# Optimization experiments

Hardware: AMD Instinct MI355X
Metric: run time of the kernel (lower is better)

The kernel has to match this reference:

```python
import jax, jax.numpy as jnp
import numpy as np

IN_FEATURES = 2048
OUT_FEATURES = 8192


def setup_inputs() -> dict:
    key = jax.random.key(0)
    k_x, k_w, k_s, k_b = jax.random.split(key, 4)
    x = jax.random.normal(k_x, (4, 2048, IN_FEATURES), dtype=jnp.float32)
    # int8 weights as produced by quantize(): values in [-128, 127]
    weight_int8 = jax.random.randint(k_w, (OUT_FEATURES, IN_FEATURES), -128, 128, dtype=jnp.int8)
    # per-output-row scale, shape [out_features, 1]
    scale = jax.random.uniform(k_s, (OUT_FEATURES, 1), dtype=jnp.float32, minval=1e-4, maxval=0.02)
    bias = jax.random.normal(k_b, (OUT_FEATURES,), dtype=jnp.float32) * 0.01
    return {"x": x, "weight_int8": weight_int8, "scale": scale, "bias": bias}


def reference(x, weight_int8, scale, bias):
    # dequantize: [out, in] int8 -> x.dtype, scaled per output row
    weight = weight_int8.astype(x.dtype) * scale.astype(x.dtype)
    # F.linear: x @ weight.T + bias
    return jnp.einsum('bsi,oi->bso', x, weight) + bias.astype(x.dtype)
```

## Files before the change

### kernel.cpp

```cpp
#include <hip/hip_runtime.h>
#include <hip/hip_bf16.h>

#define M_DIM 8192
#define N_DIM 8192
#define K_DIM 2048

#define BK 64
#define NT (K_DIM / BK)
#define SLOT_BYTES 32768

typedef float f32x4 __attribute__((ext_vector_type(4)));
typedef int   i32x4 __attribute__((ext_vector_type(4)));
typedef unsigned int u32;
typedef u32 u32x2 __attribute__((ext_vector_type(2)));
typedef u32 u32x4 __attribute__((ext_vector_type(4)));


__device__ __forceinline__ void gload16(const unsigned char* g, char* l) {
    __builtin_amdgcn_global_load_lds(
        (const __attribute__((address_space(1))) u32*)g,
        (__attribute__((address_space(3))) u32*)l, 16, 0, 0);
}

__device__ __forceinline__ u32 pack4(int a, int b, int c, int d) {
    return (u32)(a & 255) | ((u32)(b & 255) << 8) |
           ((u32)(c & 255) << 16) | ((u32)(d & 255) << 24);
}


__global__ void __launch_bounds__(256) quant_x_k(const float* __restrict__ x,
                                                 unsigned char* __restrict__ xq,
                                                 float* __restrict__ sx) {
    const int row = blockIdx.x;
    const int t = threadIdx.x;
    const float* xr = x + (size_t)row * K_DIM;
    f32x4 v0 = *((const f32x4*)xr + t * 2);
    f32x4 v1 = *((const f32x4*)xr + t * 2 + 1);
    float m = fabsf(v0[0]);
    m = fmaxf(m, fabsf(v0[1])); m = fmaxf(m, fabsf(v0[2])); m = fmaxf(m, fabsf(v0[3]));
    m = fmaxf(m, fabsf(v1[0])); m = fmaxf(m, fabsf(v1[1]));
    m = fmaxf(m, fabsf(v1[2])); m = fmaxf(m, fabsf(v1[3]));
#pragma unroll
    for (int off = 32; off >= 1; off >>= 1)
        m = fmaxf(m, __shfl_xor(m, off, 64));
    __shared__ float wmax[4];
    if ((t & 63) == 0) wmax[t >> 6] = m;
    __syncthreads();
    m = fmaxf(fmaxf(wmax[0], wmax[1]), fmaxf(wmax[2], wmax[3]));
    m = fmaxf(m, 1e-20f);
    const float rs = 127.0f / m;
    const int q0 = (int)rintf(v0[0] * rs), q1 = (int)rintf(v0[1] * rs);
    const int q2 = (int)rintf(v0[2] * rs), q3 = (int)rintf(v0[3] * rs);
    const int q4 = (int)rintf(v1[0] * rs), q5 = (int)rintf(v1[1] * rs);
    const int q6 = (int)rintf(v1[2] * rs), q7 = (int)rintf(v1[3] * rs);
    u32x2 o;
    o[0] = pack4(q0, q1, q2, q3);
    o[1] = pack4(q4, q5, q6, q7);
    *((u32x2*)(xq + (size_t)row * K_DIM) + t) = o;
    if (t == 0) sx[row] = m / 127.0f;
}


__global__ void __launch_bounds__(256) cvt_w_k(const int* __restrict__ w,
                                               unsigned char* __restrict__ wq, int n16) {
    const int stride = gridDim.x * blockDim.x;
    for (int i = blockIdx.x * blockDim.x + threadIdx.x; i < n16; i += stride) {
        const i32x4* p = (const i32x4*)w + (size_t)i * 4;
        i32x4 a = p[0], b = p[1], c = p[2], d = p[3];
        u32x4 o;
        o[0] = pack4(a[0], a[1], a[2], a[3]);
        o[1] = pack4(b[0], b[1], b[2], b[3]);
        o[2] = pack4(c[0], c[1], c[2], c[3]);
        o[3] = pack4(d[0], d[1], d[2], d[3]);
        *((u32x4*)wq + i) = o;
    }
}


__global__ void __launch_bounds__(512, 2)
gemm_i8(const unsigned char* __restrict__ Aq, const unsigned char* __restrict__ Bq,
        const float* __restrict__ sx, const float* __restrict__ sw,
        const float* __restrict__ bias, float* __restrict__ C) {
    extern __shared__ __align__(16) char ldsb[];

    const int bid = blockIdx.x;
    const int swz = (bid & 7) * 128 + (bid >> 3);
    const int rowBase = (swz >> 5) * 256;
    const int colBase = (swz & 31) * 256;

    const int t = threadIdx.x;
    const int l = t & 63;
    const int w = t >> 6;
    const int wm = w >> 2;
    const int wn = w & 3;
    const int fr = l & 15;
    const int s4 = l >> 4;

    const int sr = t >> 2;
    const int sk = (((t & 3) ^ ((sr >> 1) & 3)) * 16);
    const unsigned char* gA0 = Aq + (size_t)(rowBase + sr) * K_DIM + sk;
    const unsigned char* gA1 = Aq + (size_t)(rowBase + 128 + sr) * K_DIM + sk;
    const unsigned char* gB0 = Bq + (size_t)(colBase + sr) * K_DIM + sk;
    const unsigned char* gB1 = Bq + (size_t)(colBase + 128 + sr) * K_DIM + sk;

#define STAGE(tk) do { \
        char* _b = ldsb + ((tk) & 3) * SLOT_BYTES; \
        const int _k = (tk) * BK; \
        gload16(gA0 + _k, _b + t * 16); \
        gload16(gA1 + _k, _b + 8192 + t * 16); \
        gload16(gB0 + _k, _b + 16384 + t * 16); \
        gload16(gB1 + _k, _b + 24576 + t * 16); \
    } while (0)

    const int pc = ((s4 ^ ((fr >> 1) & 3)) * 16);
    int aoff[8], boff[4];
#pragma unroll
    for (int mi = 0; mi < 8; ++mi)
        aoff[mi] = (wm * 128 + mi * 16 + fr) * 64 + pc;
#pragma unroll
    for (int ni = 0; ni < 4; ++ni)
        boff[ni] = 16384 + (wn * 64 + ni * 16 + fr) * 64 + pc;

    i32x4 acc[8][4] = {};
    i32x4 afC[8], bf0[4], bf1[4];

#define SB    __builtin_amdgcn_sched_barrier(0)
#define BAR   __builtin_amdgcn_s_barrier()
#define P1    __builtin_amdgcn_s_setprio(1)
#define P0    __builtin_amdgcn_s_setprio(0)
#define LGKM0 asm volatile("s_waitcnt lgkmcnt(0)" ::: "memory")
#define VM8   asm volatile("s_waitcnt vmcnt(8)" ::: "memory")
#define VM4   asm volatile("s_waitcnt vmcnt(4)" ::: "memory")
#define VM0   asm volatile("s_waitcnt vmcnt(0)" ::: "memory")

#define READS_B(dst, tk) do { \
        const char* _s = ldsb + ((tk) & 3) * SLOT_BYTES; \
        _Pragma("unroll") \
        for (int ni = 0; ni < 4; ++ni) dst[ni] = *(const i32x4*)(_s + boff[ni]); \
    } while (0)
#define READS_A(tk) do { \
        const char* _s = ldsb + ((tk) & 3) * SLOT_BYTES; \
        _Pragma("unroll") \
        for (int mi = 0; mi < 8; ++mi) afC[mi] = *(const i32x4*)(_s + aoff[mi]); \
    } while (0)
#define MFMA_ALL(BREG) do { P1; \
        _Pragma("unroll") \
        for (int mi = 0; mi < 8; ++mi) \
            _Pragma("unroll") \
            for (int ni = 0; ni < 4; ++ni) \
                acc[mi][ni] = __builtin_amdgcn_mfma_i32_16x16x64_i8( \
                    afC[mi], BREG[ni], acc[mi][ni], 0, 0, 0); \
        P0; } while (0)

#define BODY(TK, BCUR, BNXT) do { \
        STAGE((TK) + 3); \
        VM8; LGKM0; SB; BAR; SB; \
        READS_B(BNXT, (TK) + 1); SB; \
        MFMA_ALL(BCUR); SB; \
        READS_A((TK) + 1); SB; \
    } while (0)

    STAGE(0); STAGE(1); STAGE(2);
    VM8; SB; BAR; SB;
    READS_B(bf0, 0); READS_A(0); SB;

#pragma unroll 1
    for (int tk = 0; tk < NT - 4; tk += 2) {
        BODY(tk, bf0, bf1);
        BODY(tk + 1, bf1, bf0);
    }
    BODY(28, bf0, bf1);
    VM4; LGKM0; SB; BAR; SB;
    READS_B(bf0, 30); SB;
    MFMA_ALL(bf1); SB;
    READS_A(30); SB;
    VM0; LGKM0; SB; BAR; SB;
    READS_B(bf1, 31); SB;
    MFMA_ALL(bf0); SB;
    READS_A(31); SB;
    MFMA_ALL(bf1);

#undef BODY
#undef MFMA_ALL
#undef READS_A
#undef READS_B
#undef STAGE

#pragma unroll
    for (int ni = 0; ni < 4; ++ni) {
        const int col = colBase + wn * 64 + ni * 16 + fr;
        const float swc = sw[col];
        const float bz = bias[col];
#pragma unroll
        for (int mi = 0; mi < 8; ++mi) {
            const int rb = rowBase + wm * 128 + mi * 16 + s4 * 4;
            i32x4 a = acc[mi][ni];
#pragma unroll
            for (int r = 0; r < 4; ++r)
                C[(size_t)(rb + r) * N_DIM + col] =
                    (float)a[r] * (sx[rb + r] * swc) + bz;
        }
    }
}


typedef int i32x4_t __attribute__((ext_vector_type(4)));
__global__ void __launch_bounds__(256) naive_k(const float* __restrict__ x,
                                               const int* __restrict__ w,
                                               const float* __restrict__ scale,
                                               const float* __restrict__ bias,
                                               float* __restrict__ out) {
    __shared__ float xs[K_DIM];
    const int m = blockIdx.x >> 5;
    const int n = ((blockIdx.x & 31) << 8) + threadIdx.x;
    for (int i = threadIdx.x; i < K_DIM; i += 256) xs[i] = x[(size_t)m * K_DIM + i];
    __syncthreads();
    const int* wr = w + (size_t)n * K_DIM;
    float acc = 0.f;
    for (int k = 0; k < K_DIM; k += 4) {
        i32x4_t v = *(const i32x4_t*)(wr + k);
        acc += xs[k]     * (float)v[0];
        acc += xs[k + 1] * (float)v[1];
        acc += xs[k + 2] * (float)v[2];
        acc += xs[k + 3] * (float)v[3];
    }
    out[(size_t)m * N_DIM + n] = acc * scale[n] + bias[n];
}


extern "C" void kernel_launch(void* const* d_in, const int* in_sizes, int n_in,
                              void* d_out, int out_size, void* d_ws, size_t ws_size,
                              hipStream_t stream) {
    const float* x     = (const float*)d_in[0];
    const int*   w8    = (const int*)d_in[1];
    const float* sw    = (const float*)d_in[2];
    const float* bias  = (const float*)d_in[3];
    float*       out   = (float*)d_out;

    const size_t xq_bytes = (size_t)M_DIM * K_DIM;
    const size_t wq_bytes = (size_t)N_DIM * K_DIM;
    const size_t need = xq_bytes + wq_bytes + (size_t)M_DIM * sizeof(float);
    if (ws_size >= need) {
        unsigned char* xq = (unsigned char*)d_ws;
        unsigned char* wq = xq + xq_bytes;
        float* sx = (float*)(wq + wq_bytes);
        hipFuncSetAttribute((const void*)gemm_i8,
                            hipFuncAttributeMaxDynamicSharedMemorySize, 131072);
        quant_x_k<<<M_DIM, 256, 0, stream>>>(x, xq, sx);
        cvt_w_k<<<2048, 256, 0, stream>>>(w8, wq, N_DIM * K_DIM / 16);
        gemm_i8<<<dim3((M_DIM / 256) * (N_DIM / 256)), 512, 131072, stream>>>(
            xq, wq, sx, sw, bias, out);
    } else {
        naive_k<<<(M_DIM * (N_DIM / 256)), 256, 0, stream>>>(x, w8, sw, bias, out);
    }
}
```

Before: 220.7 us.

## Shrink GEMM tile to 128x256 with double-buffered LDS and higher occupancy

Halves the M tile of the int8 GEMM from 256 to 128 rows, cutting per-block accumulators and LDS use. The pipeline drops from 4 LDS slots to 2, with a simpler stage/read/MFMA loop, and launch bounds now ask for 4 blocks per CU instead of 2. The aim is to raise occupancy and hide latency through more resident waves. In exchange, arithmetic intensity per block drops, global traffic for B roughly doubles, and the loop adds an extra barrier per iteration.

```diff
diff --git a/kernel.cpp b/kernel.cpp
--- a/kernel.cpp
+++ b/kernel.cpp
@@ -7,7 +7,7 @@
 
 #define BK 64
 #define NT (K_DIM / BK)
-#define SLOT_BYTES 32768
+#define SLOT_BYTES 24576
 
 typedef float f32x4 __attribute__((ext_vector_type(4)));
 typedef int   i32x4 __attribute__((ext_vector_type(4)));
@@ -77,15 +77,15 @@
 }
 
 
-__global__ void __launch_bounds__(512, 2)
+__global__ void __launch_bounds__(512, 4)
 gemm_i8(const unsigned char* __restrict__ Aq, const unsigned char* __restrict__ Bq,
         const float* __restrict__ sx, const float* __restrict__ sw,
         const float* __restrict__ bias, float* __restrict__ C) {
     extern __shared__ __align__(16) char ldsb[];
 
     const int bid = blockIdx.x;
-    const int swz = (bid & 7) * 128 + (bid >> 3);
-    const int rowBase = (swz >> 5) * 256;
+    const int swz = (bid & 7) * 256 + (bid >> 3);
+    const int rowBase = (swz >> 5) * 128;
     const int colBase = (swz & 31) * 256;
 
     const int t = threadIdx.x;
@@ -99,91 +99,75 @@
     const int sr = t >> 2;
     const int sk = (((t & 3) ^ ((sr >> 1) & 3)) * 16);
     const unsigned char* gA0 = Aq + (size_t)(rowBase + sr) * K_DIM + sk;
-    const unsigned char* gA1 = Aq + (size_t)(rowBase + 128 + sr) * K_DIM + sk;
     const unsigned char* gB0 = Bq + (size_t)(colBase + sr) * K_DIM + sk;
     const unsigned char* gB1 = Bq + (size_t)(colBase + 128 + sr) * K_DIM + sk;
 
 #define STAGE(tk) do { \
-        char* _b = ldsb + ((tk) & 3) * SLOT_BYTES; \
+        char* _b = ldsb + ((tk) & 1) * SLOT_BYTES; \
         const int _k = (tk) * BK; \
         gload16(gA0 + _k, _b + t * 16); \
-        gload16(gA1 + _k, _b + 8192 + t * 16); \
-        gload16(gB0 + _k, _b + 16384 + t * 16); \
-        gload16(gB1 + _k, _b + 24576 + t * 16); \
+        gload16(gB0 + _k, _b + 8192 + t * 16); \
+        gload16(gB1 + _k, _b + 16384 + t * 16); \
     } while (0)
 
     const int pc = ((s4 ^ ((fr >> 1) & 3)) * 16);
-    int aoff[8], boff[4];
-#pragma unroll
-    for (int mi = 0; mi < 8; ++mi)
-        aoff[mi] = (wm * 128 + mi * 16 + fr) * 64 + pc;
+    int aoff[4], boff[4];
+#pragma unroll
+    for (int mi = 0; mi < 4; ++mi)
+        aoff[mi] = (wm * 64 + mi * 16 + fr) * 64 + pc;
 #pragma unroll
     for (int ni = 0; ni < 4; ++ni)
-        boff[ni] = 16384 + (wn * 64 + ni * 16 + fr) * 64 + pc;
-
-    i32x4 acc[8][4] = {};
-    i32x4 afC[8], bf0[4], bf1[4];
+        boff[ni] = 8192 + (wn * 64 + ni * 16 + fr) * 64 + pc;
+
+    i32x4 acc[4][4] = {};
+    i32x4 af[4], bf[4];
 
 #define SB    __builtin_amdgcn_sched_barrier(0)
 #define BAR   __builtin_amdgcn_s_barrier()
 #define P1    __builtin_amdgcn_s_setprio(1)
 #define P0    __builtin_amdgcn_s_setprio(0)
 #define LGKM0 asm volatile("s_waitcnt lgkmcnt(0)" ::: "memory")
-#define VM8   asm volatile("s_waitcnt vmcnt(8)" ::: "memory")
-#define VM4   asm volatile("s_waitcnt vmcnt(4)" ::: "memory")
+#define VM3   asm volatile("s_waitcnt vmcnt(3)" ::: "memory")
 #define VM0   asm volatile("s_waitcnt vmcnt(0)" ::: "memory")
 
-#define READS_B(dst, tk) do { \
-        const char* _s = ldsb + ((tk) & 3) * SLOT_BYTES; \
+#define READS(tk) do { \
+        const char* _s = ldsb + ((tk) & 1) * SLOT_BYTES; \
         _Pragma("unroll") \
-        for (int ni = 0; ni < 4; ++ni) dst[ni] = *(const i32x4*)(_s + boff[ni]); \
+        for (int mi = 0; mi < 4; ++mi) af[mi] = *(const i32x4*)(_s + aoff[mi]); \
+        _Pragma("unroll") \
+        for (int ni = 0; ni < 4; ++ni) bf[ni] = *(const i32x4*)(_s + boff[ni]); \
     } while (0)
-#define READS_A(tk) do { \
-        const char* _s = ldsb + ((tk) & 3) * SLOT_BYTES; \
+
+#define MFMA16 do { P1; \
         _Pragma("unroll") \
-        for (int mi = 0; mi < 8; ++mi) afC[mi] = *(const i32x4*)(_s + aoff[mi]); \
-    } while (0)
-#define MFMA_ALL(BREG) do { P1; \
-        _Pragma("unroll") \
-        for (int mi = 0; mi < 8; ++mi) \
+        for (int mi = 0; mi < 4; ++mi) \
             _Pragma("unroll") \
             for (int ni = 0; ni < 4; ++ni) \
                 acc[mi][ni] = __builtin_amdgcn_mfma_i32_16x16x64_i8( \
-                    afC[mi], BREG[ni], acc[mi][ni], 0, 0, 0); \
+                    af[mi], bf[ni], acc[mi][ni], 0, 0, 0); \
         P0; } while (0)
 
-#define BODY(TK, BCUR, BNXT) do { \
-        STAGE((TK) + 3); \
-        VM8; LGKM0; SB; BAR; SB; \
-        READS_B(BNXT, (TK) + 1); SB; \
-        MFMA_ALL(BCUR); SB; \
-        READS_A((TK) + 1); SB; \
-    } while (0)
-
-    STAGE(0); STAGE(1); STAGE(2);
-    VM8; SB; BAR; SB;
-    READS_B(bf0, 0); READS_A(0); SB;
-
-#pragma unroll 1
-    for (int tk = 0; tk < NT - 4; tk += 2) {
-        BODY(tk, bf0, bf1);
-        BODY(tk + 1, bf1, bf0);
-    }
-    BODY(28, bf0, bf1);
-    VM4; LGKM0; SB; BAR; SB;
-    READS_B(bf0, 30); SB;
-    MFMA_ALL(bf1); SB;
-    READS_A(30); SB;
-    VM0; LGKM0; SB; BAR; SB;
-    READS_B(bf1, 31); SB;
-    MFMA_ALL(bf0); SB;
-    READS_A(31); SB;
-    MFMA_ALL(bf1);
-
-#undef BODY
-#undef MFMA_ALL
-#undef READS_A
-#undef READS_B
+    STAGE(0); STAGE(1);
+    VM3; SB; BAR; SB;
+
+#pragma unroll
+    for (int tk = 0; tk < NT - 2; ++tk) {
+        READS(tk);
+        LGKM0; SB; BAR; SB;
+        STAGE(tk + 2);
+        MFMA16;
+        VM3; SB; BAR; SB;
+    }
+    READS(NT - 2);
+    LGKM0; SB; BAR; SB;
+    MFMA16;
+    VM0; SB; BAR; SB;
+    READS(NT - 1);
+    LGKM0; SB;
+    MFMA16;
+
+#undef MFMA16
+#undef READS
 #undef STAGE
 
 #pragma unroll
@@ -192,8 +176,8 @@
         const float swc = sw[col];
         const float bz = bias[col];
 #pragma unroll
-        for (int mi = 0; mi < 8; ++mi) {
-            const int rb = rowBase + wm * 128 + mi * 16 + s4 * 4;
+        for (int mi = 0; mi < 4; ++mi) {
+            const int rb = rowBase + wm * 64 + mi * 16 + s4 * 4;
             i32x4 a = acc[mi][ni];
 #pragma unroll
             for (int r = 0; r < 4; ++r)
@@ -245,10 +229,10 @@
         unsigned char* wq = xq + xq_bytes;
         float* sx = (float*)(wq + wq_bytes);
         hipFuncSetAttribute((const void*)gemm_i8,
-                            hipFuncAttributeMaxDynamicSharedMemorySize, 131072);
+                            hipFuncAttributeMaxDynamicSharedMemorySize, 2 * SLOT_BYTES);
         quant_x_k<<<M_DIM, 256, 0, stream>>>(x, xq, sx);
         cvt_w_k<<<2048, 256, 0, stream>>>(w8, wq, N_DIM * K_DIM / 16);
-        gemm_i8<<<dim3((M_DIM / 256) * (N_DIM / 256)), 512, 131072, stream>>>(
+        gemm_i8<<<dim3((M_DIM / 128) * (N_DIM / 256)), 512, 2 * SLOT_BYTES, stream>>>(
             xq, wq, sx, sw, bias, out);
     } else {
         naive_k<<<(M_DIM * (N_DIM / 256)), 256, 0, stream>>>(x, w8, sw, bias, out);
```

After: 245.1 us. 11.1% more time.

## Double-buffer A and B fragments and restructure the LDS pipeline schedule

Applied to the files above, without the earlier changes.

Register fragments for both A and B are now double-buffered. Each step issues the LDS reads for the next tile before running the 32 MFMAs on the current one, so LDS latency hides behind matrix work. The prefetch distance drops from three tiles to two, with a single barrier per step, and the main loop is fully unrolled. This raises VGPR pressure with 24 extra vector registers, which may lower occupancy. The shorter prefetch distance also exposes more global-load latency.

```diff
diff --git a/kernel.cpp b/kernel.cpp
--- a/kernel.cpp
+++ b/kernel.cpp
@@ -122,68 +122,62 @@
         boff[ni] = 16384 + (wn * 64 + ni * 16 + fr) * 64 + pc;
 
     i32x4 acc[8][4] = {};
-    i32x4 afC[8], bf0[4], bf1[4];
+    i32x4 af0[8], bf0[4], af1[8], bf1[4];
 
 #define SB    __builtin_amdgcn_sched_barrier(0)
 #define BAR   __builtin_amdgcn_s_barrier()
 #define P1    __builtin_amdgcn_s_setprio(1)
 #define P0    __builtin_amdgcn_s_setprio(0)
 #define LGKM0 asm volatile("s_waitcnt lgkmcnt(0)" ::: "memory")
-#define VM8   asm volatile("s_waitcnt vmcnt(8)" ::: "memory")
 #define VM4   asm volatile("s_waitcnt vmcnt(4)" ::: "memory")
 #define VM0   asm volatile("s_waitcnt vmcnt(0)" ::: "memory")
 
-#define READS_B(dst, tk) do { \
-        const char* _s = ldsb + ((tk) & 3) * SLOT_BYTES; \
+#define READS(T, AF, BF) do { \
+        const char* _s = ldsb + ((T) & 3) * SLOT_BYTES; \
         _Pragma("unroll") \
-        for (int ni = 0; ni < 4; ++ni) dst[ni] = *(const i32x4*)(_s + boff[ni]); \
+        for (int mi = 0; mi < 8; ++mi) AF[mi] = *(const i32x4*)(_s + aoff[mi]); \
+        _Pragma("unroll") \
+        for (int ni = 0; ni < 4; ++ni) BF[ni] = *(const i32x4*)(_s + boff[ni]); \
     } while (0)
-#define READS_A(tk) do { \
-        const char* _s = ldsb + ((tk) & 3) * SLOT_BYTES; \
-        _Pragma("unroll") \
-        for (int mi = 0; mi < 8; ++mi) afC[mi] = *(const i32x4*)(_s + aoff[mi]); \
-    } while (0)
-#define MFMA_ALL(BREG) do { P1; \
+
+#define MFMA32(AF, BF) do { P1; \
         _Pragma("unroll") \
         for (int mi = 0; mi < 8; ++mi) \
             _Pragma("unroll") \
             for (int ni = 0; ni < 4; ++ni) \
                 acc[mi][ni] = __builtin_amdgcn_mfma_i32_16x16x64_i8( \
-                    afC[mi], BREG[ni], acc[mi][ni], 0, 0, 0); \
+                    AF[mi], BF[ni], acc[mi][ni], 0, 0, 0); \
         P0; } while (0)
 
-#define BODY(TK, BCUR, BNXT) do { \
-        STAGE((TK) + 3); \
-        VM8; LGKM0; SB; BAR; SB; \
-        READS_B(BNXT, (TK) + 1); SB; \
-        MFMA_ALL(BCUR); SB; \
-        READS_A((TK) + 1); SB; \
+#define BODY(T, AC, BC, AN, BN, DOSTAGE, VMW) do { \
+        READS(T, AN, BN); \
+        if (DOSTAGE) STAGE((T) + 2); \
+        SB; \
+        MFMA32(AC, BC); \
+        VMW; LGKM0; SB; BAR; SB; \
     } while (0)
 
     STAGE(0); STAGE(1); STAGE(2);
-    VM8; SB; BAR; SB;
-    READS_B(bf0, 0); READS_A(0); SB;
-
-#pragma unroll 1
-    for (int tk = 0; tk < NT - 4; tk += 2) {
-        BODY(tk, bf0, bf1);
-        BODY(tk + 1, bf1, bf0);
-    }
-    BODY(28, bf0, bf1);
-    VM4; LGKM0; SB; BAR; SB;
-    READS_B(bf0, 30); SB;
-    MFMA_ALL(bf1); SB;
-    READS_A(30); SB;
-    VM0; LGKM0; SB; BAR; SB;
-    READS_B(bf1, 31); SB;
-    MFMA_ALL(bf0); SB;
-    READS_A(31); SB;
-    MFMA_ALL(bf1);
+    VM4; SB; BAR; SB;
+    READS(0, af0, bf0);
+    LGKM0; SB;
+
+#pragma unroll
+    for (int tt = 1; tt <= 27; tt += 2) {
+        BODY(tt,     af0, bf0, af1, bf1, true, VM4);
+        BODY(tt + 1, af1, bf1, af0, bf0, true, VM4);
+    }
+    BODY(29, af0, bf0, af1, bf1, true,  VM4);
+    BODY(30, af1, bf1, af0, bf0, false, VM0);
+    READS(31, af1, bf1);
+    SB;
+    MFMA32(af0, bf0);
+    LGKM0; SB;
+    MFMA32(af1, bf1);
 
 #undef BODY
-#undef MFMA_ALL
-#undef READS_A
-#undef READS_B
+#undef MFMA32
+#undef READS
 #undef STAGE
 
 #pragma unroll
```

Measured after the change: 235.9 us. +6.9%, slower.
